# Kernel tuning notes

Measured on AMD Instinct MI355X. Metric: run time of the kernel, lower is better.

Reference implementation:

```python
import jax, jax.numpy as jnp
import numpy as np

B, S, N = 8, 4096, 512
K_DIM, HEADS, WS = 512, 8, 128
HD = K_DIM // HEADS


def setup_inputs() -> dict:
    key = jax.random.key(0)
    ks = jax.random.split(key, 9)
    sc = 0.02
    return {
        "inputs": jax.random.normal(ks[0], (B, S, N), dtype=jnp.float32),
        "Wq": jax.random.normal(ks[1], (K_DIM, N), dtype=jnp.float32) * sc,
        "bq": jax.random.normal(ks[2], (K_DIM,), dtype=jnp.float32) * sc,
        "Wk": jax.random.normal(ks[3], (K_DIM, N), dtype=jnp.float32) * sc,
        "bk": jax.random.normal(ks[4], (K_DIM,), dtype=jnp.float32) * sc,
        "Wv": jax.random.normal(ks[5], (K_DIM, N), dtype=jnp.float32) * sc,
        "bv": jax.random.normal(ks[6], (K_DIM,), dtype=jnp.float32) * sc,
        "Wp": jax.random.normal(ks[7], (N, K_DIM), dtype=jnp.float32) * sc,
        "bp": jax.random.normal(ks[8], (N,), dtype=jnp.float32) * sc,
    }


def reference(inputs, Wq, bq, Wk, bk, Wv, bv, Wp, bp):
    b, s, n = inputs.shape
    nw = s // WS  # number of windows per sequence
    # QKV projections (torch Linear: x @ W.T + b)
    q = inputs @ Wq.T + bq  # [B,S,K]
    k = inputs @ Wk.T + bk
    v = inputs @ Wv.T + bv

    def to_windows(t):
        # [B,S,K] -> [B*nw, H, WS, HD]
        t = t.reshape(b * nw, WS, HEADS, HD)
        return t.transpose(0, 2, 1, 3)

    q, k, v = to_windows(q), to_windows(k), to_windows(v)
    scale = HD ** (-0.5)
    # windowed attention: [BW,H,WS,WS]
    score = jnp.einsum('whqd,whkd->whqk', q, k) * scale
    attn = jax.nn.softmax(score, axis=-1)  # dropout is identity in eval
    out = jnp.einsum('whqk,whkd->whqd', attn, v)  # [BW,H,WS,HD]
    out = out.transpose(0, 2, 1, 3).reshape(b, s, K_DIM)  # window reverse
    out = out @ Wp.T + bp  # [B,S,N]
    return out
```

## Files before the change

kernel.cpp:

```cpp
#include <hip/hip_runtime.h>
#include <hip/hip_bf16.h>
#include <stdint.h>


typedef __bf16 bf16;
typedef __bf16 bf16x8 __attribute__((ext_vector_type(8)));
typedef __bf16 bf16x4 __attribute__((ext_vector_type(4)));
typedef __bf16 bf16x2 __attribute__((ext_vector_type(2)));
typedef float  f32x4  __attribute__((ext_vector_type(4)));
typedef float  f32x16 __attribute__((ext_vector_type(16)));

#define DEV static __device__ __forceinline__

DEV void gld_lds16(const bf16* g, bf16* l) {
  __builtin_amdgcn_global_load_lds(
      (__attribute__((address_space(1))) void*)(g),
      (__attribute__((address_space(3))) void*)(l), 16, 0, 0);
}

__global__ void cast_all(const float* __restrict__ x,
                         const float* __restrict__ Wq, const float* __restrict__ Wk,
                         const float* __restrict__ Wv, const float* __restrict__ Wp,
                         bf16* __restrict__ xb, bf16* __restrict__ wb) {
  int i = blockIdx.x * blockDim.x + threadIdx.x;
  const float* src;
  bf16* dst;
  if (i < 4194304) {
    src = x + i * 4;
    dst = xb + i * 4;
  } else {
    int e = (i - 4194304) * 4;
    int off;
    const float* w;
    if (e < 786432) {
      int seg = e >> 18;
      off = e & 262143;
      w = (seg == 0) ? Wq : ((seg == 1) ? Wk : Wv);
    } else {
      off = e - 786432;
      w = Wp;
    }
    src = w + off;
    dst = wb + e;
  }
  float4 v = *(const float4*)src;
  bf16x4 o;
  o[0] = (bf16)v.x; o[1] = (bf16)v.y; o[2] = (bf16)v.z; o[3] = (bf16)v.w;
  *(bf16x4*)dst = o;
}

template <bool BF16OUT, int NCOL>
__global__ __launch_bounds__(256, 4)
void gemm_bt(const bf16* __restrict__ A, const bf16* __restrict__ B,
             const float* __restrict__ bias0, const float* __restrict__ bias1,
             const float* __restrict__ bias2, void* __restrict__ Cout) {
  constexpr int Ntot = NCOL * 128;
  __shared__ bf16 As[128 * 64];
  __shared__ bf16 Bs[128 * 64];
  const int tid = threadIdx.x;
  const int wave = tid >> 6, lane = tid & 63;
  const int wm = wave >> 1, wn = wave & 1;
  const int lane31 = lane & 31, khalf = lane >> 5;

  const int nb = gridDim.x;
  const int j = blockIdx.x;
  const int l = (j & 7) * (nb >> 3) + (j >> 3);
  const long row0 = (long)(l / NCOL) * 128;
  const long col0 = (long)(l % NCOL) * 128;

  f32x16 acc[2][2] = {};

  const int srow = lane >> 3;
  const int sg = (lane & 7) ^ srow;

  for (int k0 = 0; k0 < 512; k0 += 64) {
    __syncthreads();
    for (int i = 0; i < 4; ++i) {
      int r0 = (wave * 4 + i) * 8;
      gld_lds16(A + (row0 + r0 + srow) * 512 + k0 + sg * 8, As + r0 * 64 + lane * 8);
      gld_lds16(B + (col0 + r0 + srow) * 512 + k0 + sg * 8, Bs + r0 * 64 + lane * 8);
    }
    __syncthreads();
    for (int s = 0; s < 4; ++s) {
      bf16x8 af[2], bfr[2];
      for (int r = 0; r < 2; ++r) {
        int row = wm * 64 + r * 32 + lane31;
        int ph = (s * 2 + khalf) ^ (row & 7);
        af[r] = *(const bf16x8*)(As + row * 64 + ph * 8);
      }
      for (int c = 0; c < 2; ++c) {
        int row = wn * 64 + c * 32 + lane31;
        int ph = (s * 2 + khalf) ^ (row & 7);
        bfr[c] = *(const bf16x8*)(Bs + row * 64 + ph * 8);
      }
      for (int r = 0; r < 2; ++r)
        for (int c = 0; c < 2; ++c)
          acc[r][c] = __builtin_amdgcn_mfma_f32_32x32x16_bf16(af[r], bfr[c], acc[r][c], 0, 0, 0);
    }
  }

  for (int r = 0; r < 2; ++r) {
    for (int c = 0; c < 2; ++c) {
      long col = col0 + wn * 64 + c * 32 + lane31;
      int seg = (int)(col >> 9);
      const float* bsel = (seg == 0) ? bias0 : ((seg == 1) ? bias1 : bias2);
      float bias = bsel[col & 511];
      for (int reg = 0; reg < 16; ++reg) {
        int rr = (reg & 3) + 8 * (reg >> 2) + 4 * khalf;
        long row = row0 + wm * 64 + r * 32 + rr;
        float v = acc[r][c][reg] + bias;
        if (BF16OUT) ((bf16*)Cout)[row * Ntot + col] = (bf16)v;
        else        ((float*)Cout)[row * Ntot + col] = v;
      }
    }
  }
}

__global__ __launch_bounds__(512, 4)
void attn_win(const bf16* __restrict__ QKV, bf16* __restrict__ Out) {
  __shared__ __align__(16) char smem[49152];
  bf16* Qs = (bf16*)smem;
  bf16* Ks = Qs + 128 * 64;
  bf16* Ps = (bf16*)smem;
  bf16* Vt = (bf16*)(smem + 32768);

  const int tid = threadIdx.x;
  const int wave = tid >> 6, lane = tid & 63;
  const int lane15 = lane & 15, quad = lane >> 4;
  const int win = blockIdx.x >> 3, head = blockIdx.x & 7;

  const bf16* Qg = QKV + (size_t)win * 128 * 1536 + head * 64;
  const bf16* Kg = Qg + 512;
  const bf16* Vg = Qg + 1024;

  {
    const int srow = lane >> 3;
    const int sg = (lane & 7) ^ srow;
    for (int i = 0; i < 2; ++i) {
      int r0 = (wave * 2 + i) * 8;
      gld_lds16(Qg + (size_t)(r0 + srow) * 1536 + sg * 8, Qs + r0 * 64 + lane * 8);
      gld_lds16(Kg + (size_t)(r0 + srow) * 1536 + sg * 8, Ks + r0 * 64 + lane * 8);
    }
  }
  {
    int tp = tid >> 3;
    int d0 = (tid & 7) * 8;
    bf16x8 v0 = *(const bf16x8*)(Vg + (size_t)(2 * tp) * 1536 + d0);
    bf16x8 v1 = *(const bf16x8*)(Vg + (size_t)(2 * tp + 1) * 1536 + d0);
    int gt = tp >> 2, po = tp & 3;
    for (int j = 0; j < 8; ++j) {
      int d = d0 + j;
      int p = gt ^ ((d >> 3) ^ (d & 7));
      bf16x2 pr;
      pr[0] = v0[j]; pr[1] = v1[j];
      *(bf16x2*)(Vt + d * 128 + p * 8 + po * 2) = pr;
    }
  }
  __syncthreads();

  f32x4 accs[8] = {};
  {
    bf16x8 aq[2];
    for (int s = 0; s < 2; ++s) {
      int row = wave * 16 + lane15;
      aq[s] = *(const bf16x8*)(Qs + row * 64 + (((s * 4 + quad) ^ (lane15 & 7)) * 8));
    }
    for (int c = 0; c < 8; ++c) {
      int row = c * 16 + lane15;
      for (int s = 0; s < 2; ++s) {
        bf16x8 bk = *(const bf16x8*)(Ks + row * 64 + (((s * 4 + quad) ^ (lane15 & 7)) * 8));
        accs[c] = __builtin_amdgcn_mfma_f32_16x16x32_bf16(aq[s], bk, accs[c], 0, 0, 0);
      }
    }
  }
  __syncthreads();

  const float scale = 0.125f;
  for (int g = 0; g < 4; ++g) {
    float sum = 0.f;
    for (int c = 0; c < 8; ++c) {
      float e = __expf(accs[c][g] * scale);
      accs[c][g] = e;
      sum += e;
    }
    for (int mk = 1; mk <= 8; mk <<= 1) sum += __shfl_xor(sum, mk, 64);
    float inv = 1.0f / sum;
    int prow = wave * 16 + quad * 4 + g;
    int rsw = prow & 7;
    for (int c = 0; c < 8; ++c) {
      int col = c * 16 + lane15;
      int p = (col >> 3) ^ rsw;
      Ps[prow * 128 + p * 8 + (col & 7)] = (bf16)(accs[c][g] * inv);
    }
  }
  __syncthreads();

  f32x4 acco[4] = {};
  for (int kk = 0; kk < 4; ++kk) {
    int arow = wave * 16 + lane15;
    int pa = (kk * 4 + quad) ^ (arow & 7);
    bf16x8 a = *(const bf16x8*)(Ps + arow * 128 + pa * 8);
    for (int c = 0; c < 4; ++c) {
      int d = c * 16 + lane15;
      int p = (kk * 4 + quad) ^ ((d >> 3) ^ (d & 7));
      bf16x8 b = *(const bf16x8*)(Vt + d * 128 + p * 8);
      acco[c] = __builtin_amdgcn_mfma_f32_16x16x32_bf16(a, b, acco[c], 0, 0, 0);
    }
  }

  bf16* Og = Out + (size_t)win * 128 * 512 + head * 64;
  {
    int row = wave * 16 + quad * 4;
    for (int c = 0; c < 4; ++c) {
      int col = c * 16 + lane15;
      for (int g = 0; g < 4; ++g)
        Og[(size_t)(row + g) * 512 + col] = (bf16)acco[c][g];
    }
  }
}

extern "C" void kernel_launch(void* const* d_in, const int* in_sizes, int n_in,
                              void* d_out, int out_size, void* d_ws, size_t ws_size,
                              hipStream_t stream) {
  const float* x  = (const float*)d_in[0];
  const float* Wq = (const float*)d_in[1];
  const float* bq = (const float*)d_in[2];
  const float* Wk = (const float*)d_in[3];
  const float* bk = (const float*)d_in[4];
  const float* Wv = (const float*)d_in[5];
  const float* bv = (const float*)d_in[6];
  const float* Wp = (const float*)d_in[7];
  const float* bp = (const float*)d_in[8];

  bf16* Xb    = (bf16*)d_ws;
  bf16* Wqkvb = Xb + 16777216;
  bf16* Wpb   = Wqkvb + 786432;
  bf16* QKVb  = Wpb + 262144;
  bf16* AttnB = QKVb + 50331648;

  cast_all<<<17408, 256, 0, stream>>>(x, Wq, Wk, Wv, Wp, Xb, Wqkvb);
  gemm_bt<true, 12><<<3072, 256, 0, stream>>>(Xb, Wqkvb, bq, bk, bv, QKVb);
  attn_win<<<2048, 512, 0, stream>>>(QKVb, AttnB);
  gemm_bt<false, 4><<<1024, 256, 0, stream>>>(AttnB, Wpb, bp, bp, bp, d_out);
}
```

Measured before the change: 254.9 us.

## Replace GEMMs with 256x256-tile double-buffered 8-wave kernel using quadrant MMA scheduling

Both projection GEMMs move from 128x128 tiles on 4 waves to 256x256 tiles on 8 waves. Global-to-LDS loads are double-buffered with explicit vmcnt waits, and the k-loop is split into four quadrant MFMA phases separated by barriers, with s_setprio raised around the MFMAs. The aim is more data reuse per block and overlap of loads with compute. In exchange it uses 128KB of LDS and more registers per thread, and launches far fewer blocks (768 and 256), which may underfill the CUs.

```diff
diff --git a/kernel.cpp b/kernel.cpp
--- a/kernel.cpp
+++ b/kernel.cpp
@@ -8,7 +8,6 @@
 typedef __bf16 bf16x4 __attribute__((ext_vector_type(4)));
 typedef __bf16 bf16x2 __attribute__((ext_vector_type(2)));
 typedef float  f32x4  __attribute__((ext_vector_type(4)));
-typedef float  f32x16 __attribute__((ext_vector_type(16)));
 
 #define DEV static __device__ __forceinline__
 
@@ -49,68 +48,135 @@
   *(bf16x4*)dst = o;
 }
 
-template <bool BF16OUT, int NCOL>
-__global__ __launch_bounds__(256, 4)
-void gemm_bt(const bf16* __restrict__ A, const bf16* __restrict__ B,
+template <bool BF16OUT, int NTILES>
+__global__ __launch_bounds__(512, 2)
+void gemm256(const bf16* __restrict__ A, const bf16* __restrict__ B,
              const float* __restrict__ bias0, const float* __restrict__ bias1,
              const float* __restrict__ bias2, void* __restrict__ Cout) {
-  constexpr int Ntot = NCOL * 128;
-  __shared__ bf16 As[128 * 64];
-  __shared__ bf16 Bs[128 * 64];
+  constexpr int Ntot = NTILES * 256;
+  __shared__ __align__(16) bf16 smem[2][2][256 * 64];
+
   const int tid = threadIdx.x;
   const int wave = tid >> 6, lane = tid & 63;
-  const int wm = wave >> 1, wn = wave & 1;
-  const int lane31 = lane & 31, khalf = lane >> 5;
+  const int wm = wave >> 2, wn = wave & 3;
+  const int lane15 = lane & 15, kq = lane >> 4;
+  const int srow = lane >> 3, sg = (lane & 7) ^ srow;
 
   const int nb = gridDim.x;
   const int j = blockIdx.x;
   const int l = (j & 7) * (nb >> 3) + (j >> 3);
-  const long row0 = (long)(l / NCOL) * 128;
-  const long col0 = (long)(l % NCOL) * 128;
-
-  f32x16 acc[2][2] = {};
-
-  const int srow = lane >> 3;
-  const int sg = (lane & 7) ^ srow;
-
-  for (int k0 = 0; k0 < 512; k0 += 64) {
-    __syncthreads();
-    for (int i = 0; i < 4; ++i) {
-      int r0 = (wave * 4 + i) * 8;
-      gld_lds16(A + (row0 + r0 + srow) * 512 + k0 + sg * 8, As + r0 * 64 + lane * 8);
-      gld_lds16(B + (col0 + r0 + srow) * 512 + k0 + sg * 8, Bs + r0 * 64 + lane * 8);
-    }
-    __syncthreads();
-    for (int s = 0; s < 4; ++s) {
-      bf16x8 af[2], bfr[2];
-      for (int r = 0; r < 2; ++r) {
-        int row = wm * 64 + r * 32 + lane31;
-        int ph = (s * 2 + khalf) ^ (row & 7);
-        af[r] = *(const bf16x8*)(As + row * 64 + ph * 8);
+  const long row0 = (long)(l / NTILES) * 256;
+  const long col0 = (long)(l % NTILES) * 256;
+
+  f32x4 acc[8][4] = {};
+  bf16x8 af[4][2], bfr[2][2];
+
+#define STAGE(T, BUF)                                                          \
+  {                                                                            \
+    const long kb_ = (long)(T) * 64;                                           \
+    _Pragma("unroll") for (int i_ = 0; i_ < 4; ++i_) {                         \
+      const int r0_ = wave * 32 + i_ * 8;                                      \
+      gld_lds16(A + (row0 + r0_ + srow) * 512 + kb_ + sg * 8,                  \
+                &smem[BUF][0][r0_ * 64]);                                      \
+      gld_lds16(B + (col0 + r0_ + srow) * 512 + kb_ + sg * 8,                  \
+                &smem[BUF][1][r0_ * 64]);                                      \
+    }                                                                          \
+  }
+
+#define READ_A(QM, BUF)                                                        \
+  {                                                                            \
+    _Pragma("unroll") for (int mt_ = 0; mt_ < 4; ++mt_) {                      \
+      const int r_ = wm * 128 + (QM) * 64 + mt_ * 16 + lane15;                 \
+      const bf16* p_ = &smem[BUF][0][r_ * 64];                                 \
+      _Pragma("unroll") for (int ks_ = 0; ks_ < 2; ++ks_) {                    \
+        const int c_ = (ks_ * 4 + kq) ^ (r_ & 7);                              \
+        af[mt_][ks_] = *(const bf16x8*)(p_ + c_ * 8);                          \
+      }                                                                        \
+    }                                                                          \
+  }
+
+#define READ_B(QN, BUF)                                                        \
+  {                                                                            \
+    _Pragma("unroll") for (int nt_ = 0; nt_ < 2; ++nt_) {                      \
+      const int r_ = wn * 64 + (QN) * 32 + nt_ * 16 + lane15;                  \
+      const bf16* p_ = &smem[BUF][1][r_ * 64];                                 \
+      _Pragma("unroll") for (int ks_ = 0; ks_ < 2; ++ks_) {                    \
+        const int c_ = (ks_ * 4 + kq) ^ (r_ & 7);                              \
+        bfr[nt_][ks_] = *(const bf16x8*)(p_ + c_ * 8);                         \
+      }                                                                        \
+    }                                                                          \
+  }
+
+#define MMA_Q(QM, QN)                                                          \
+  {                                                                            \
+    __builtin_amdgcn_s_setprio(1);                                             \
+    _Pragma("unroll") for (int mt_ = 0; mt_ < 4; ++mt_)                        \
+    _Pragma("unroll") for (int nt_ = 0; nt_ < 2; ++nt_)                        \
+    _Pragma("unroll") for (int ks_ = 0; ks_ < 2; ++ks_)                        \
+      acc[(QM) * 4 + mt_][(QN) * 2 + nt_] =                                    \
+          __builtin_amdgcn_mfma_f32_16x16x32_bf16(                             \
+              af[mt_][ks_], bfr[nt_][ks_],                                     \
+              acc[(QM) * 4 + mt_][(QN) * 2 + nt_], 0, 0, 0);                   \
+    __builtin_amdgcn_s_setprio(0);                                             \
+  }
+
+  STAGE(0, 0);
+  STAGE(1, 1);
+  asm volatile("s_waitcnt vmcnt(8)" ::: "memory");
+  __builtin_amdgcn_s_barrier();
+
+  for (int kt = 0; kt < 8; ++kt) {
+    const int cur = kt & 1;
+    READ_A(0, cur); READ_B(0, cur);
+    __builtin_amdgcn_s_barrier();
+    MMA_Q(0, 0);
+    __builtin_amdgcn_s_barrier();
+    READ_B(1, cur);
+    __builtin_amdgcn_s_barrier();
+    MMA_Q(0, 1);
+    __builtin_amdgcn_s_barrier();
+    READ_A(1, cur);
+    __builtin_amdgcn_s_barrier();
+    MMA_Q(1, 1);
+    __builtin_amdgcn_s_barrier();
+    READ_B(0, cur);
+    __builtin_amdgcn_s_barrier();
+    MMA_Q(1, 0);
+    __builtin_amdgcn_s_barrier();
+
+    if (kt + 2 < 8) {
+      STAGE(kt + 2, cur);
+      asm volatile("s_waitcnt vmcnt(8)" ::: "memory");
+      __builtin_amdgcn_s_barrier();
+    } else if (kt + 1 < 8) {
+      asm volatile("s_waitcnt vmcnt(0)" ::: "memory");
+      __builtin_amdgcn_s_barrier();
+    }
+  }
+
+#undef STAGE
+#undef READ_A
+#undef READ_B
+#undef MMA_Q
+
+  const long crow = row0 + wm * 128;
+  const long ccol = col0 + wn * 64;
+  for (int m = 0; m < 8; ++m) {
+    for (int n = 0; n < 4; ++n) {
+      const long col = ccol + n * 16 + lane15;
+      const float* bsel;
+      if (NTILES == 6) {
+        const int seg = (int)(col >> 9);
+        bsel = (seg == 0) ? bias0 : ((seg == 1) ? bias1 : bias2);
+      } else {
+        bsel = bias0;
       }
-      for (int c = 0; c < 2; ++c) {
-        int row = wn * 64 + c * 32 + lane31;
-        int ph = (s * 2 + khalf) ^ (row & 7);
-        bfr[c] = *(const bf16x8*)(Bs + row * 64 + ph * 8);
-      }
-      for (int r = 0; r < 2; ++r)
-        for (int c = 0; c < 2; ++c)
-          acc[r][c] = __builtin_amdgcn_mfma_f32_32x32x16_bf16(af[r], bfr[c], acc[r][c], 0, 0, 0);
-    }
-  }
-
-  for (int r = 0; r < 2; ++r) {
-    for (int c = 0; c < 2; ++c) {
-      long col = col0 + wn * 64 + c * 32 + lane31;
-      int seg = (int)(col >> 9);
-      const float* bsel = (seg == 0) ? bias0 : ((seg == 1) ? bias1 : bias2);
-      float bias = bsel[col & 511];
-      for (int reg = 0; reg < 16; ++reg) {
-        int rr = (reg & 3) + 8 * (reg >> 2) + 4 * khalf;
-        long row = row0 + wm * 64 + r * 32 + rr;
-        float v = acc[r][c][reg] + bias;
-        if (BF16OUT) ((bf16*)Cout)[row * Ntot + col] = (bf16)v;
-        else        ((float*)Cout)[row * Ntot + col] = v;
+      const float bias = bsel[col & 511];
+      const long row = crow + m * 16 + kq * 4;
+      for (int g = 0; g < 4; ++g) {
+        const float v = acc[m][n][g] + bias;
+        if (BF16OUT) ((bf16*)Cout)[(row + g) * Ntot + col] = (bf16)v;
+        else         ((float*)Cout)[(row + g) * Ntot + col] = v;
       }
     }
   }
@@ -239,7 +305,7 @@
   bf16* AttnB = QKVb + 50331648;
 
   cast_all<<<17408, 256, 0, stream>>>(x, Wq, Wk, Wv, Wp, Xb, Wqkvb);
-  gemm_bt<true, 12><<<3072, 256, 0, stream>>>(Xb, Wqkvb, bq, bk, bv, QKVb);
+  gemm256<true, 6><<<768, 512, 0, stream>>>(Xb, Wqkvb, bq, bk, bv, QKVb);
   attn_win<<<2048, 512, 0, stream>>>(QKVb, AttnB);
-  gemm_bt<false, 4><<<1024, 256, 0, stream>>>(AttnB, Wpb, bp, bp, bp, d_out);
-}
+  gemm256<false, 2><<<256, 512, 0, stream>>>(AttnB, Wpb, bp, bp, bp, d_out);
+}
```

Result: no change. 252.5 us (-0.9%).
